# Kernel tuning notes

Hardware: AMD Instinct MI355X
Metric: run time of the kernel (lower is better)

Reference implementation:

```python
import jax, jax.numpy as jnp
import numpy as np

RETURN_SHAPE = (128, 128)


def dht2(x):
    # Discrete Hartley Transform over the spatial axes (2, 3):
    # H = Re(FFT) - Im(FFT). Unnormalized, matching scipy.fft default.
    f = jnp.fft.fftn(x, axes=(2, 3))
    return f.real - f.imag


def setup_inputs() -> dict:
    key = jax.random.key(0)
    x = jax.random.normal(key, (8, 64, 256, 256), dtype=jnp.float32)
    return {"x": x}


def reference(x) -> jnp.ndarray:
    # Spectral pooling: DHT -> center crop in frequency domain -> DHT.
    h_out, w_out = RETURN_SHAPE
    H, W = x.shape[2], x.shape[3]
    d = dht2(x)
    sh = (H - h_out) // 2
    sw = (W - w_out) // 2
    cropped = d[:, :, sh:sh + h_out, sw:sw + w_out]
    return dht2(cropped).astype(jnp.float32)
```

## Files before the change

kernel.cpp:

```cpp
#include <hip/hip_runtime.h>
#include <math.h>


typedef __attribute__((ext_vector_type(8))) short bfrag;
typedef __attribute__((ext_vector_type(4))) float ffrag;

#define PI2_256 0.0245436926061702597f
#define PI2_128 0.0490873852123405194f

__device__ __forceinline__ unsigned short f2bf(float f) {
    union { float f; unsigned int u; } v; v.f = f;
    unsigned int r = v.u + 0x7fffu + ((v.u >> 16) & 1u);
    return (unsigned short)(r >> 16);
}

__device__ __forceinline__ bfrag pack8(float4 a, float4 b) {
    bfrag r;
    r[0] = (short)f2bf(a.x); r[1] = (short)f2bf(a.y);
    r[2] = (short)f2bf(a.z); r[3] = (short)f2bf(a.w);
    r[4] = (short)f2bf(b.x); r[5] = (short)f2bf(b.y);
    r[6] = (short)f2bf(b.z); r[7] = (short)f2bf(b.w);
    return r;
}

__global__ __launch_bounds__(256) void gen_tables(unsigned short* __restrict__ ws)
{
    const int id = blockIdx.x * 256 + threadIdx.x;
    {
        const int j = id >> 8, m = id & 255;
        const int mult = (j < 128) ? (64 + j) : (320 - j);
        const int idx = (mult * m) & 255;
        float s, c; sincosf((float)idx * PI2_256, &s, &c);
        ws[id] = f2bf(c + s);
    }
    {
        const int u = id >> 9, k = id & 511;
        const int up = 64 + u;
        float s, c, val;
        if (k < 256) { sincosf((float)((up * k) & 255) * PI2_256, &s, &c); val = c; }
        else         { sincosf((float)((up * (k - 256)) & 255) * PI2_256, &s, &c); val = s; }
        ws[65536 + id] = f2bf(val);
    }
    if (id < 32768) {
        {
            const int j = id >> 7, m = id & 127;
            const int mult = (j < 128) ? j : (256 - j);
            const int idx = (mult * m) & 127;
            float s, c; sincosf((float)idx * PI2_128, &s, &c);
            ws[131072 + id] = f2bf(c + s);
        }
        {
            const int u = id >> 8, k = id & 255;
            float s, c, val;
            if (k < 128) { sincosf((float)((u * k) & 127) * PI2_128, &s, &c); val = c; }
            else         { sincosf((float)((u * (k - 128)) & 127) * PI2_128, &s, &c); val = s; }
            ws[163840 + id] = f2bf(val);
        }
    }
}

__global__ __launch_bounds__(512, 2) void stage1(const float* __restrict__ X,
                                                 const unsigned short* __restrict__ ws,
                                                 float* __restrict__ dc)
{
    __shared__ unsigned short PQt[128 * 512];

    const int t  = threadIdx.x;
    const int w  = t >> 6;
    const int ln = t & 15;
    const int q  = (t & 63) >> 4;
    const int img = blockIdx.x;

    const float* __restrict__ Xi = X + (size_t)img * 65536;
    const unsigned short* __restrict__ W1 = ws;
    const unsigned short* __restrict__ W2 = ws + 65536;

    {
        ffrag acc[2][16];
#pragma unroll
        for (int mt = 0; mt < 2; ++mt)
#pragma unroll
            for (int nt = 0; nt < 16; ++nt)
                acc[mt][nt] = (ffrag){0.f, 0.f, 0.f, 0.f};

        const int rowA0 = 32 * w;
        for (int kk = 0; kk < 8; ++kk) {
            const int k = kk * 32 + q * 8;
            bfrag A[2];
#pragma unroll
            for (int mt = 0; mt < 2; ++mt) {
                const float* xp = Xi + (size_t)(rowA0 + 16 * mt + ln) * 256 + k;
                const float4 x0 = *(const float4*)xp;
                const float4 x1 = *(const float4*)(xp + 4);
                A[mt] = pack8(x0, x1);
            }
#pragma unroll
            for (int nt = 0; nt < 16; ++nt) {
                const int j = nt * 16 + ln;
                const bfrag B = *(const bfrag*)(W1 + j * 256 + k);
#pragma unroll
                for (int mt = 0; mt < 2; ++mt)
                    acc[mt][nt] = __builtin_amdgcn_mfma_f32_16x16x32_bf16(A[mt], B, acc[mt][nt], 0, 0, 0);
            }
        }
#pragma unroll
        for (int mt = 0; mt < 2; ++mt) {
#pragma unroll
            for (int nt = 0; nt < 16; ++nt) {
                const int c  = nt * 16 + ln;
                const int v  = c & 127;
                const int kb = ((c < 128) ? 0 : 256) + rowA0 + 16 * mt + 4 * q;
                const unsigned int lo = (unsigned int)f2bf(acc[mt][nt][0]) |
                                        ((unsigned int)f2bf(acc[mt][nt][1]) << 16);
                const unsigned int hi = (unsigned int)f2bf(acc[mt][nt][2]) |
                                        ((unsigned int)f2bf(acc[mt][nt][3]) << 16);
                const int phys = v * 512 + ((((kb >> 3) ^ (v & 7)) << 3)) + (kb & 7);
                *(uint2*)&PQt[phys] = make_uint2(lo, hi);
            }
        }
    }
    __syncthreads();

    {
        ffrag acc[8];
#pragma unroll
        for (int nt = 0; nt < 8; ++nt) acc[nt] = (ffrag){0.f, 0.f, 0.f, 0.f};

        const int u0 = 16 * w;
        for (int kk = 0; kk < 16; ++kk) {
            const int k = kk * 32 + q * 8;
            const bfrag A = *(const bfrag*)(W2 + (size_t)(u0 + ln) * 512 + k);
#pragma unroll
            for (int nt = 0; nt < 8; ++nt) {
                const int v = nt * 16 + ln;
                const int g = (k >> 3) ^ (v & 7);
                const bfrag B = *(const bfrag*)&PQt[v * 512 + (g << 3)];
                acc[nt] = __builtin_amdgcn_mfma_f32_16x16x32_bf16(A, B, acc[nt], 0, 0, 0);
            }
        }
        float* __restrict__ D = dc + (size_t)img * 16384;
#pragma unroll
        for (int nt = 0; nt < 8; ++nt) {
#pragma unroll
            for (int r = 0; r < 4; ++r) {
                const int u = u0 + 4 * q + r;
                const int v = nt * 16 + ln;
                D[u * 128 + v] = acc[nt][r];
            }
        }
    }
}

__global__ __launch_bounds__(256, 2) void stage2(const unsigned short* __restrict__ ws,
                                                 float* __restrict__ io)
{
    __shared__ unsigned short Dcb[128 * 128];
    __shared__ unsigned short PQ2[64 * 256];

    const int t  = threadIdx.x;
    const int w  = t >> 6;
    const int ln = t & 15;
    const int q  = (t & 63) >> 4;
    const int img = blockIdx.x;

    float* __restrict__ G = io + (size_t)img * 16384;
    const unsigned short* __restrict__ W3 = ws + 131072;
    const unsigned short* __restrict__ W4 = ws + 163840;

    {
        const int p = t >> 1, half = t & 1;
        const float* src = G + p * 128 + half * 64;
#pragma unroll
        for (int g = 0; g < 8; ++g) {
            const float4 a = *(const float4*)(src + g * 8);
            const float4 b = *(const float4*)(src + g * 8 + 4);
            const int m0 = half * 64 + g * 8;
            const int gran = (m0 >> 3) ^ (p & 7);
            uint4 val;
            val.x = (unsigned int)f2bf(a.x) | ((unsigned int)f2bf(a.y) << 16);
            val.y = (unsigned int)f2bf(a.z) | ((unsigned int)f2bf(a.w) << 16);
            val.z = (unsigned int)f2bf(b.x) | ((unsigned int)f2bf(b.y) << 16);
            val.w = (unsigned int)f2bf(b.z) | ((unsigned int)f2bf(b.w) << 16);
            *(uint4*)&Dcb[p * 128 + gran * 8] = val;
        }
    }
    __syncthreads();

    for (int vh = 0; vh < 2; ++vh) {
        ffrag acc[2][8];
#pragma unroll
        for (int mt = 0; mt < 2; ++mt)
#pragma unroll
            for (int nt = 0; nt < 8; ++nt)
                acc[mt][nt] = (ffrag){0.f, 0.f, 0.f, 0.f};

        const int p0 = 32 * w;
        for (int kk = 0; kk < 4; ++kk) {
            const int k = kk * 32 + q * 8;
            bfrag A[2];
#pragma unroll
            for (int mt = 0; mt < 2; ++mt) {
                const int p = p0 + 16 * mt + ln;
                const int g = (k >> 3) ^ (p & 7);
                A[mt] = *(const bfrag*)&Dcb[p * 128 + g * 8];
            }
#pragma unroll
            for (int nt = 0; nt < 8; ++nt) {
                const int c = nt * 16 + ln;
                const int j = (c < 64) ? (64 * vh + c) : (128 + 64 * vh + (c - 64));
                const bfrag B = *(const bfrag*)(W3 + j * 128 + k);
#pragma unroll
                for (int mt = 0; mt < 2; ++mt)
                    acc[mt][nt] = __builtin_amdgcn_mfma_f32_16x16x32_bf16(A[mt], B, acc[mt][nt], 0, 0, 0);
            }
        }
        __syncthreads();
#pragma unroll
        for (int mt = 0; mt < 2; ++mt) {
#pragma unroll
            for (int nt = 0; nt < 8; ++nt) {
                const int c  = nt * 16 + ln;
                const int v  = c & 63;
                const int kb = ((c < 64) ? 0 : 128) + p0 + 16 * mt + 4 * q;
                const unsigned int lo = (unsigned int)f2bf(acc[mt][nt][0]) |
                                        ((unsigned int)f2bf(acc[mt][nt][1]) << 16);
                const unsigned int hi = (unsigned int)f2bf(acc[mt][nt][2]) |
                                        ((unsigned int)f2bf(acc[mt][nt][3]) << 16);
                const int phys = v * 256 + ((((kb >> 3) ^ (v & 7)) << 3)) + (kb & 7);
                *(uint2*)&PQ2[phys] = make_uint2(lo, hi);
            }
        }
        __syncthreads();

        ffrag o[2][4];
#pragma unroll
        for (int mt = 0; mt < 2; ++mt)
#pragma unroll
            for (int nt = 0; nt < 4; ++nt)
                o[mt][nt] = (ffrag){0.f, 0.f, 0.f, 0.f};

        const int u0 = 32 * w;
        for (int kk = 0; kk < 8; ++kk) {
            const int k = kk * 32 + q * 8;
            bfrag A[2];
#pragma unroll
            for (int mt = 0; mt < 2; ++mt)
                A[mt] = *(const bfrag*)(W4 + (size_t)(u0 + 16 * mt + ln) * 256 + k);
#pragma unroll
            for (int nt = 0; nt < 4; ++nt) {
                const int v = nt * 16 + ln;
                const int g = (k >> 3) ^ (v & 7);
                const bfrag B = *(const bfrag*)&PQ2[v * 256 + (g << 3)];
#pragma unroll
                for (int mt = 0; mt < 2; ++mt)
                    o[mt][nt] = __builtin_amdgcn_mfma_f32_16x16x32_bf16(A[mt], B, o[mt][nt], 0, 0, 0);
            }
        }
#pragma unroll
        for (int mt = 0; mt < 2; ++mt) {
#pragma unroll
            for (int nt = 0; nt < 4; ++nt) {
#pragma unroll
                for (int r = 0; r < 4; ++r) {
                    const int u = u0 + 16 * mt + 4 * q + r;
                    const int v = 64 * vh + nt * 16 + ln;
                    G[u * 128 + v] = o[mt][nt][r];
                }
            }
        }
    }
}

extern "C" void kernel_launch(void* const* d_in, const int* in_sizes, int n_in,
                              void* d_out, int out_size, void* d_ws, size_t ws_size,
                              hipStream_t stream)
{
    const float* x = (const float*)d_in[0];
    float* out = (float*)d_out;
    unsigned short* tw = (unsigned short*)d_ws;

    gen_tables<<<dim3(256), dim3(256), 0, stream>>>(tw);
    stage1<<<dim3(512), dim3(512), 0, stream>>>(x, tw, out);
    stage2<<<dim3(512), dim3(256), 0, stream>>>(tw, out);
}
```

Measured before the change: 275.9 us.

## Split fused DHT stages into four GEMM passes with LDS-staged twiddle tables

```diff
diff --git a/kernel.cpp b/kernel.cpp
--- a/kernel.cpp
+++ b/kernel.cpp
@@ -23,6 +23,34 @@
     return r;
 }
 
+__device__ __forceinline__ uint2 packlohi(ffrag a) {
+    uint2 r;
+    r.x = (unsigned int)f2bf(a[0]) | ((unsigned int)f2bf(a[1]) << 16);
+    r.y = (unsigned int)f2bf(a[2]) | ((unsigned int)f2bf(a[3]) << 16);
+    return r;
+}
+
+template<int NCOLS, int K>
+__device__ __forceinline__ void stageB(const unsigned short* __restrict__ src,
+                                       unsigned short* __restrict__ Lb, int t)
+{
+    constexpr int CHUNKS = NCOLS * K / 8;
+#pragma unroll
+    for (int i = 0; i < CHUNKS / 512; ++i) {
+        const int o = (t + i * 512) * 8;
+        const int j = o / K;
+        const int k = o - j * K;
+        const uint4 v = *(const uint4*)(src + o);
+        *(uint4*)&Lb[j * K + (((k >> 3) ^ (j & 7)) << 3)] = v;
+    }
+}
+
+template<int K>
+__device__ __forceinline__ bfrag ldsB(const unsigned short* __restrict__ Lb, int j, int k)
+{
+    return *(const bfrag*)&Lb[j * K + (((k >> 3) ^ (j & 7)) << 3)];
+}
+
 __global__ __launch_bounds__(256) void gen_tables(unsigned short* __restrict__ ws)
 {
     const int id = blockIdx.x * 256 + threadIdx.x;
@@ -59,9 +87,173 @@
     }
 }
 
-__global__ __launch_bounds__(512, 2) void stage1(const float* __restrict__ X,
-                                                 const unsigned short* __restrict__ ws,
-                                                 float* __restrict__ dc)
+__global__ __launch_bounds__(512, 2) void pass1(const float* __restrict__ X,
+                                                const unsigned short* __restrict__ ws,
+                                                unsigned short* __restrict__ Ct)
+{
+    __shared__ unsigned short Lb[256 * 256];
+
+    const int t  = threadIdx.x;
+    const int w  = t >> 6;
+    const int ln = t & 15;
+    const int q  = (t & 63) >> 4;
+
+    stageB<256, 256>(ws, Lb, t);
+    __syncthreads();
+
+    const int img = blockIdx.x >> 1;
+    const int nb  = (blockIdx.x & 1) * 128;
+    const float* __restrict__ Ar = X + (size_t)img * 65536 + (size_t)(nb + 16 * w + ln) * 256;
+
+    ffrag acc[16];
+#pragma unroll
+    for (int nt = 0; nt < 16; ++nt) acc[nt] = (ffrag){0.f, 0.f, 0.f, 0.f};
+
+    for (int kk = 0; kk < 8; ++kk) {
+        const int k = kk * 32 + q * 8;
+        const float4 x0 = *(const float4*)(Ar + k);
+        const float4 x1 = *(const float4*)(Ar + k + 4);
+        const bfrag A = pack8(x0, x1);
+#pragma unroll
+        for (int nt = 0; nt < 16; ++nt) {
+            const bfrag B = ldsB<256>(Lb, nt * 16 + ln, k);
+            acc[nt] = __builtin_amdgcn_mfma_f32_16x16x32_bf16(A, B, acc[nt], 0, 0, 0);
+        }
+    }
+    unsigned short* __restrict__ Co = Ct + (size_t)img * 65536 + nb + 16 * w + 4 * q;
+#pragma unroll
+    for (int nt = 0; nt < 16; ++nt) {
+        *(uint2*)&Co[(size_t)(nt * 16 + ln) * 256] = packlohi(acc[nt]);
+    }
+}
+
+__global__ __launch_bounds__(512, 2) void pass2(const unsigned short* __restrict__ Ct,
+                                                const unsigned short* __restrict__ ws,
+                                                unsigned short* __restrict__ Dc)
+{
+    __shared__ unsigned short Lb[128 * 512];
+
+    const int t  = threadIdx.x;
+    const int w  = t >> 6;
+    const int ln = t & 15;
+    const int q  = (t & 63) >> 4;
+
+    stageB<128, 512>(ws + 65536, Lb, t);
+    __syncthreads();
+
+    const int img = blockIdx.x;
+    const unsigned short* __restrict__ Abase = Ct + (size_t)img * 65536;
+    const int v = 16 * w + ln;
+
+    ffrag acc[8];
+#pragma unroll
+    for (int nt = 0; nt < 8; ++nt) acc[nt] = (ffrag){0.f, 0.f, 0.f, 0.f};
+
+#pragma unroll
+    for (int kh = 0; kh < 2; ++kh) {
+        const unsigned short* __restrict__ Ar = Abase + (size_t)(v + kh * 128) * 256;
+        for (int kk = 0; kk < 8; ++kk) {
+            const int k = kk * 32 + q * 8;
+            const bfrag A = *(const bfrag*)(Ar + k);
+            const int kfull = kh * 256 + k;
+#pragma unroll
+            for (int nt = 0; nt < 8; ++nt) {
+                const bfrag B = ldsB<512>(Lb, nt * 16 + ln, kfull);
+                acc[nt] = __builtin_amdgcn_mfma_f32_16x16x32_bf16(A, B, acc[nt], 0, 0, 0);
+            }
+        }
+    }
+    unsigned short* __restrict__ Do = Dc + (size_t)img * 16384 + 16 * w + 4 * q;
+#pragma unroll
+    for (int nt = 0; nt < 8; ++nt) {
+        *(uint2*)&Do[(size_t)(nt * 16 + ln) * 128] = packlohi(acc[nt]);
+    }
+}
+
+__global__ __launch_bounds__(512, 2) void pass3(const unsigned short* __restrict__ Dc,
+                                                const unsigned short* __restrict__ ws,
+                                                unsigned short* __restrict__ C3t)
+{
+    __shared__ unsigned short Lb[256 * 128];
+
+    const int t  = threadIdx.x;
+    const int w  = t >> 6;
+    const int ln = t & 15;
+    const int q  = (t & 63) >> 4;
+
+    stageB<256, 128>(ws + 131072, Lb, t);
+    __syncthreads();
+
+    const int img = blockIdx.x;
+    const unsigned short* __restrict__ Ar = Dc + (size_t)img * 16384 + (size_t)(16 * w + ln) * 128;
+
+    ffrag acc[16];
+#pragma unroll
+    for (int nt = 0; nt < 16; ++nt) acc[nt] = (ffrag){0.f, 0.f, 0.f, 0.f};
+
+    for (int kk = 0; kk < 4; ++kk) {
+        const int k = kk * 32 + q * 8;
+        const bfrag A = *(const bfrag*)(Ar + k);
+#pragma unroll
+        for (int nt = 0; nt < 16; ++nt) {
+            const bfrag B = ldsB<128>(Lb, nt * 16 + ln, k);
+            acc[nt] = __builtin_amdgcn_mfma_f32_16x16x32_bf16(A, B, acc[nt], 0, 0, 0);
+        }
+    }
+    unsigned short* __restrict__ Co = C3t + (size_t)img * 32768 + 16 * w + 4 * q;
+#pragma unroll
+    for (int nt = 0; nt < 16; ++nt) {
+        *(uint2*)&Co[(size_t)(nt * 16 + ln) * 128] = packlohi(acc[nt]);
+    }
+}
+
+__global__ __launch_bounds__(512, 2) void pass4(const unsigned short* __restrict__ C3t,
+                                                const unsigned short* __restrict__ ws,
+                                                float* __restrict__ out)
+{
+    __shared__ unsigned short Lb[128 * 256];
+
+    const int t  = threadIdx.x;
+    const int w  = t >> 6;
+    const int ln = t & 15;
+    const int q  = (t & 63) >> 4;
+
+    stageB<128, 256>(ws + 163840, Lb, t);
+    __syncthreads();
+
+    const int img = blockIdx.x;
+    const unsigned short* __restrict__ Abase = C3t + (size_t)img * 32768;
+    const int v = 16 * w + ln;
+
+    ffrag acc[8];
+#pragma unroll
+    for (int nt = 0; nt < 8; ++nt) acc[nt] = (ffrag){0.f, 0.f, 0.f, 0.f};
+
+#pragma unroll
+    for (int kh = 0; kh < 2; ++kh) {
+        const unsigned short* __restrict__ Ar = Abase + (size_t)(v + kh * 128) * 128;
+        for (int kk = 0; kk < 4; ++kk) {
+            const int k = kk * 32 + q * 8;
+            const bfrag A = *(const bfrag*)(Ar + k);
+            const int kfull = kh * 128 + k;
+#pragma unroll
+            for (int nt = 0; nt < 8; ++nt) {
+                const bfrag B = ldsB<256>(Lb, nt * 16 + ln, kfull);
+                acc[nt] = __builtin_amdgcn_mfma_f32_16x16x32_bf16(A, B, acc[nt], 0, 0, 0);
+            }
+        }
+    }
+    float* __restrict__ G = out + (size_t)img * 16384 + 16 * w + 4 * q;
+#pragma unroll
+    for (int nt = 0; nt < 8; ++nt) {
+        float4 o4 = make_float4(acc[nt][0], acc[nt][1], acc[nt][2], acc[nt][3]);
+        *(float4*)&G[(size_t)(nt * 16 + ln) * 128] = o4;
+    }
+}
+
+__global__ __launch_bounds__(512, 2) void stage1_old(const float* __restrict__ X,
+                                                     const unsigned short* __restrict__ ws,
+                                                     float* __restrict__ dc)
 {
     __shared__ unsigned short PQt[128 * 512];
 
@@ -110,12 +302,9 @@
                 const int c  = nt * 16 + ln;
                 const int v  = c & 127;
                 const int kb = ((c < 128) ? 0 : 256) + rowA0 + 16 * mt + 4 * q;
-                const unsigned int lo = (unsigned int)f2bf(acc[mt][nt][0]) |
-                                        ((unsigned int)f2bf(acc[mt][nt][1]) << 16);
-                const unsigned int hi = (unsigned int)f2bf(acc[mt][nt][2]) |
-                                        ((unsigned int)f2bf(acc[mt][nt][3]) << 16);
-                const int phys = v * 512 + ((((kb >> 3) ^ (v & 7)) << 3)) + (kb & 7);
-                *(uint2*)&PQt[phys] = make_uint2(lo, hi);
+                const uint2 lohi = packlohi(acc[mt][nt]);
+                const int phys = v * 512 + (((kb >> 3) ^ (v & 7)) << 3) + (kb & 7);
+                *(uint2*)&PQt[phys] = lohi;
             }
         }
     }
@@ -151,8 +340,8 @@
     }
 }
 
-__global__ __launch_bounds__(256, 2) void stage2(const unsigned short* __restrict__ ws,
-                                                 float* __restrict__ io)
+__global__ __launch_bounds__(256, 2) void stage2_old(const unsigned short* __restrict__ ws,
+                                                     float* __restrict__ io)
 {
     __shared__ unsigned short Dcb[128 * 128];
     __shared__ unsigned short PQ2[64 * 256];
@@ -222,12 +411,9 @@
                 const int c  = nt * 16 + ln;
                 const int v  = c & 63;
                 const int kb = ((c < 64) ? 0 : 128) + p0 + 16 * mt + 4 * q;
-                const unsigned int lo = (unsigned int)f2bf(acc[mt][nt][0]) |
-                                        ((unsigned int)f2bf(acc[mt][nt][1]) << 16);
-                const unsigned int hi = (unsigned int)f2bf(acc[mt][nt][2]) |
-                                        ((unsigned int)f2bf(acc[mt][nt][3]) << 16);
-                const int phys = v * 256 + ((((kb >> 3) ^ (v & 7)) << 3)) + (kb & 7);
-                *(uint2*)&PQ2[phys] = make_uint2(lo, hi);
+                const uint2 lohi = packlohi(acc[mt][nt]);
+                const int phys = v * 256 + (((kb >> 3) ^ (v & 7)) << 3) + (kb & 7);
+                *(uint2*)&PQ2[phys] = lohi;
             }
         }
         __syncthreads();
@@ -280,6 +466,24 @@
     unsigned short* tw = (unsigned short*)d_ws;
 
     gen_tables<<<dim3(256), dim3(256), 0, stream>>>(tw);
-    stage1<<<dim3(512), dim3(512), 0, stream>>>(x, tw, out);
-    stage2<<<dim3(512), dim3(256), 0, stream>>>(tw, out);
-}
+
+    int G = 512;
+    while (G > 1 && (size_t)163840 * (size_t)G + 393216 > ws_size) G >>= 1;
+
+    if ((size_t)163840 * (size_t)G + 393216 <= ws_size) {
+        unsigned short* regA  = tw + 196608;
+        unsigned short* regDc = regA + (size_t)G * 65536;
+        const int nchunks = 512 / G;
+        for (int ci = 0; ci < nchunks; ++ci) {
+            const float* xc = x + (size_t)ci * G * 65536;
+            float* oc = out + (size_t)ci * G * 16384;
+            pass1<<<dim3(2 * G), dim3(512), 0, stream>>>(xc, tw, regA);
+            pass2<<<dim3(G), dim3(512), 0, stream>>>(regA, tw, regDc);
+            pass3<<<dim3(G), dim3(512), 0, stream>>>(regDc, tw, regA);
+            pass4<<<dim3(G), dim3(512), 0, stream>>>(regA, tw, oc);
+        }
+    } else {
+        stage1_old<<<dim3(512), dim3(512), 0, stream>>>(x, tw, out);
+        stage2_old<<<dim3(512), dim3(256), 0, stream>>>(tw, out);
+    }
+}
```

After: 279.1 us. About the same (+1.1%).
